# Kernel optimization log

Hardware: AMD Instinct MI355X
Metric: run time of the kernel (lower is better)

## Reference

```python
import jax, jax.numpy as jnp
import numpy as np

D_INPUT = 2048
DD_DIM = 512
DD_PAIRS = DD_DIM // 2


def setup_inputs() -> dict:
    key = jax.random.key(0)
    k1, k2, k3 = jax.random.split(key, 3)
    x = jax.random.normal(k1, (4, 4096, D_INPUT), dtype=jnp.float32)
    # Learned projection (zeros at init in torch; use small random for a non-trivial test)
    W = jax.random.normal(k2, (DD_PAIRS, D_INPUT), dtype=jnp.float32) * 0.02
    b = jax.random.normal(k3, (DD_PAIRS,), dtype=jnp.float32) * 0.02
    return {"x": x, "W": W, "b": b}


def reference(x, W, b):
    # x: (B, T, D); W: (P, D); b: (P,) with P = DD_DIM // 2
    deltas = jnp.einsum('btd,pd->btp', x, W) + b          # (B, T, P)
    angles = jnp.cumsum(deltas, axis=1)                   # cumulative phase
    cos, sin = jnp.cos(angles), jnp.sin(angles)
    x1 = x[..., :DD_PAIRS]                                # (B, T, P)
    x2 = x[..., DD_PAIRS:DD_DIM]                          # (B, T, P)
    rotated = jnp.concatenate([x1 * cos - x2 * sin, x2 * cos + x1 * sin], axis=-1)
    return jnp.concatenate([rotated, x[..., DD_DIM:]], axis=-1)
```

## Files before the change

kernel.cpp:

```cpp
#include <hip/hip_runtime.h>
#include <math.h>

#define BB 4
#define TT 4096
#define DDIM 2048
#define PP 256
#define MM (BB*TT)
#define KKDIM 2048
#define CHUNK 32
#define NCHUNK (TT/CHUNK)

typedef __attribute__((ext_vector_type(8))) short short8;
typedef __attribute__((ext_vector_type(4))) float f32x4;

__device__ __forceinline__ unsigned short f2bf(float f) {
    unsigned u = __float_as_uint(f);
    u += 0x7FFF + ((u >> 16) & 1);
    return (unsigned short)(u >> 16);
}
__device__ __forceinline__ float bf2f(unsigned short h) {
    return __uint_as_float(((unsigned)h) << 16);
}

#define LSTR 56

__global__ __launch_bounds__(256) void gemm_mfma_k(const float* __restrict__ x,
                                                   const float* __restrict__ W,
                                                   const float* __restrict__ bias,
                                                   float* __restrict__ delta,
                                                   float* __restrict__ csum) {
    __shared__ unsigned short Ahi[128 * LSTR];
    __shared__ unsigned short Alo[128 * LSTR];
    __shared__ unsigned short Bhi[64 * LSTR];
    __shared__ unsigned short Blo[64 * LSTR];

    const int n0   = blockIdx.x * 64;
    const int m0   = blockIdx.y * 128;
    const int tid  = threadIdx.x;
    const int w    = tid >> 6;
    const int lane = tid & 63;
    const int lm   = lane & 15;
    const int ko   = lane >> 4;

    f32x4 acc[2][4];
    #pragma unroll
    for (int i = 0; i < 2; ++i)
        #pragma unroll
        for (int j = 0; j < 4; ++j) {
            f32x4 z = {0.f, 0.f, 0.f, 0.f};
            acc[i][j] = z;
        }

    for (int k0 = 0; k0 < KKDIM; k0 += 32) {
        float4 av[4], bv[2];
        #pragma unroll
        for (int r = 0; r < 4; ++r) {
            int f = r * 256 + tid;
            av[r] = *(const float4*)(x + (size_t)(m0 + (f >> 3)) * KKDIM + k0 + ((f & 7) << 2));
        }
        #pragma unroll
        for (int r = 0; r < 2; ++r) {
            int f = r * 256 + tid;
            bv[r] = *(const float4*)(W + (size_t)(n0 + (f >> 3)) * KKDIM + k0 + ((f & 7) << 2));
        }
        __syncthreads();
        #pragma unroll
        for (int r = 0; r < 4; ++r) {
            int f = r * 256 + tid;
            int idx = (f >> 3) * LSTR + ((f & 7) << 2);
            float4 v = av[r];
            unsigned short h0 = f2bf(v.x), h1 = f2bf(v.y), h2 = f2bf(v.z), h3 = f2bf(v.w);
            unsigned short l0 = f2bf(v.x - bf2f(h0)), l1 = f2bf(v.y - bf2f(h1));
            unsigned short l2 = f2bf(v.z - bf2f(h2)), l3 = f2bf(v.w - bf2f(h3));
            uint2 hp = { (unsigned)h0 | ((unsigned)h1 << 16), (unsigned)h2 | ((unsigned)h3 << 16) };
            uint2 lp = { (unsigned)l0 | ((unsigned)l1 << 16), (unsigned)l2 | ((unsigned)l3 << 16) };
            *(uint2*)&Ahi[idx] = hp;
            *(uint2*)&Alo[idx] = lp;
        }
        #pragma unroll
        for (int r = 0; r < 2; ++r) {
            int f = r * 256 + tid;
            int idx = (f >> 3) * LSTR + ((f & 7) << 2);
            float4 v = bv[r];
            unsigned short h0 = f2bf(v.x), h1 = f2bf(v.y), h2 = f2bf(v.z), h3 = f2bf(v.w);
            unsigned short l0 = f2bf(v.x - bf2f(h0)), l1 = f2bf(v.y - bf2f(h1));
            unsigned short l2 = f2bf(v.z - bf2f(h2)), l3 = f2bf(v.w - bf2f(h3));
            uint2 hp = { (unsigned)h0 | ((unsigned)h1 << 16), (unsigned)h2 | ((unsigned)h3 << 16) };
            uint2 lp = { (unsigned)l0 | ((unsigned)l1 << 16), (unsigned)l2 | ((unsigned)l3 << 16) };
            *(uint2*)&Bhi[idx] = hp;
            *(uint2*)&Blo[idx] = lp;
        }
        __syncthreads();
        short8 ah[2], al[2], bh[4], bl[4];
        #pragma unroll
        for (int mt = 0; mt < 2; ++mt) {
            int idx = (w * 32 + mt * 16 + lm) * LSTR + ko * 8;
            ah[mt] = *(const short8*)&Ahi[idx];
            al[mt] = *(const short8*)&Alo[idx];
        }
        #pragma unroll
        for (int nt = 0; nt < 4; ++nt) {
            int idx = (nt * 16 + lm) * LSTR + ko * 8;
            bh[nt] = *(const short8*)&Bhi[idx];
            bl[nt] = *(const short8*)&Blo[idx];
        }
        #pragma unroll
        for (int mt = 0; mt < 2; ++mt)
            #pragma unroll
            for (int nt = 0; nt < 4; ++nt) {
                f32x4 c = acc[mt][nt];
                c = __builtin_amdgcn_mfma_f32_16x16x32_bf16(ah[mt], bh[nt], c, 0, 0, 0);
                c = __builtin_amdgcn_mfma_f32_16x16x32_bf16(ah[mt], bl[nt], c, 0, 0, 0);
                c = __builtin_amdgcn_mfma_f32_16x16x32_bf16(al[mt], bh[nt], c, 0, 0, 0);
                acc[mt][nt] = c;
            }
    }

    float bsv[4];
    #pragma unroll
    for (int nt = 0; nt < 4; ++nt) bsv[nt] = bias[n0 + nt * 16 + lm];

    float cs[4] = {0.f, 0.f, 0.f, 0.f};
    #pragma unroll
    for (int mt = 0; mt < 2; ++mt)
        #pragma unroll
        for (int nt = 0; nt < 4; ++nt)
            #pragma unroll
            for (int r = 0; r < 4; ++r) {
                float val = acc[mt][nt][r] + bsv[nt];
                int m = m0 + w * 32 + mt * 16 + ko * 4 + r;
                delta[(size_t)m * PP + n0 + nt * 16 + lm] = val;
                cs[nt] += val;
            }
    #pragma unroll
    for (int nt = 0; nt < 4; ++nt) {
        float s = cs[nt];
        s += __shfl_xor(s, 16);
        s += __shfl_xor(s, 32);
        if (lane < 16)
            csum[(size_t)(m0 / CHUNK + w) * PP + n0 + nt * 16 + lane] = s;
    }
}

__global__ __launch_bounds__(256) void scan_k(float* __restrict__ csum, int cstride) {
    const int idx = blockIdx.x * 256 + threadIdx.x;
    const int b = idx >> 8;
    const int p = idx & 255;
    float run = 0.f;
    for (int c0 = 0; c0 < NCHUNK; c0 += 8) {
        float v[8];
        #pragma unroll
        for (int j = 0; j < 8; ++j)
            v[j] = csum[(size_t)(b * NCHUNK + c0 + j) * cstride + p];
        #pragma unroll
        for (int j = 0; j < 8; ++j) {
            float t = v[j];
            csum[(size_t)(b * NCHUNK + c0 + j) * cstride + p] = run;
            run += t;
        }
    }
}

__global__ __launch_bounds__(256) void rotate_copy_k(const float* __restrict__ delta,
                                                     const float* __restrict__ csum,
                                                     const float* __restrict__ x,
                                                     float* __restrict__ out) {
    const int bc = blockIdx.x;
    const int p  = threadIdx.x;
    const int tbase = bc * CHUNK;
    float angle = csum[(size_t)bc * PP + p];
    for (int t = 0; t < CHUNK; ++t) {
        size_t row = (size_t)(tbase + t);
        angle += delta[row * PP + p];
        float s, co;
        sincosf(angle, &s, &co);
        float x1 = x[row * DDIM + p];
        float x2 = x[row * DDIM + PP + p];
        out[row * DDIM + p]      = x1 * co - x2 * s;
        out[row * DDIM + PP + p] = x2 * co + x1 * s;
    }
    const int half = p >> 7;
    const int q    = p & 127;
    for (int rp = 0; rp < 16; ++rp) {
        size_t row = (size_t)(tbase + rp * 2 + half);
        const float4* src = (const float4*)(x + row * DDIM + 512);
        float4*       dst = (float4*)(out + row * DDIM + 512);
        dst[q]       = src[q];
        dst[q + 128] = src[q + 128];
        dst[q + 256] = src[q + 256];
    }
}

__global__ __launch_bounds__(256) void gemm_k(const float* __restrict__ x,
                                              const float* __restrict__ W,
                                              const float* __restrict__ bias,
                                              float* __restrict__ delta,
                                              int dstride, int doff) {
    __shared__ float As[16][68];
    __shared__ float Bs[16][68];
    const int m0  = blockIdx.x * 64;
    const int n0  = blockIdx.y * 64;
    const int tid = threadIdx.x;
    const int lr  = tid >> 2;
    const int lc  = (tid & 3) << 2;
    const int tmi = tid & 15;
    const int tni = tid >> 4;
    float acc[4][4] = {};
    for (int k0 = 0; k0 < KKDIM; k0 += 16) {
        float4 a4 = *(const float4*)(x + (size_t)(m0 + lr) * KKDIM + k0 + lc);
        float4 b4 = *(const float4*)(W + (size_t)(n0 + lr) * KKDIM + k0 + lc);
        __syncthreads();
        As[lc + 0][lr] = a4.x; As[lc + 1][lr] = a4.y;
        As[lc + 2][lr] = a4.z; As[lc + 3][lr] = a4.w;
        Bs[lc + 0][lr] = b4.x; Bs[lc + 1][lr] = b4.y;
        Bs[lc + 2][lr] = b4.z; Bs[lc + 3][lr] = b4.w;
        __syncthreads();
        #pragma unroll
        for (int kk = 0; kk < 16; ++kk) {
            float4 av = *(const float4*)&As[kk][tmi * 4];
            float4 bv = *(const float4*)&Bs[kk][tni * 4];
            float am[4] = {av.x, av.y, av.z, av.w};
            float bn[4] = {bv.x, bv.y, bv.z, bv.w};
            #pragma unroll
            for (int i = 0; i < 4; ++i)
                #pragma unroll
                for (int j = 0; j < 4; ++j)
                    acc[i][j] += am[i] * bn[j];
        }
    }
    const float4 b4 = *(const float4*)(bias + n0 + tni * 4);
    #pragma unroll
    for (int i = 0; i < 4; ++i) {
        size_t m = (size_t)(m0 + tmi * 4 + i);
        float4 o;
        o.x = acc[i][0] + b4.x; o.y = acc[i][1] + b4.y;
        o.z = acc[i][2] + b4.z; o.w = acc[i][3] + b4.w;
        *(float4*)(delta + m * dstride + doff + n0 + tni * 4) = o;
    }
}

__global__ __launch_bounds__(256) void chunksum_k(const float* __restrict__ delta,
                                                  int dstride, int doff,
                                                  float* __restrict__ csum, int cstride) {
    const int bc = blockIdx.x;
    const int b  = bc / NCHUNK;
    const int c  = bc % NCHUNK;
    const int p  = threadIdx.x;
    const int tbase = b * TT + c * CHUNK;
    float s = 0.f;
    #pragma unroll 8
    for (int t = 0; t < CHUNK; ++t)
        s += delta[(size_t)(tbase + t) * dstride + doff + p];
    csum[(size_t)bc * cstride + p] = s;
}

__global__ __launch_bounds__(256) void rotate_k(const float* __restrict__ delta,
                                                int dstride, int doff,
                                                const float* __restrict__ csum, int cstride,
                                                const float* __restrict__ x,
                                                float* __restrict__ out) {
    const int bc = blockIdx.x;
    const int b  = bc / NCHUNK;
    const int c  = bc % NCHUNK;
    const int p  = threadIdx.x;
    const int tbase = b * TT + c * CHUNK;
    float angle = csum[(size_t)bc * cstride + p];
    for (int t = 0; t < CHUNK; ++t) {
        size_t row = (size_t)(tbase + t);
        angle += delta[row * dstride + doff + p];
        float s, co;
        sincosf(angle, &s, &co);
        float x1 = x[row * DDIM + p];
        float x2 = x[row * DDIM + PP + p];
        out[row * DDIM + p]      = x1 * co - x2 * s;
        out[row * DDIM + PP + p] = x2 * co + x1 * s;
    }
}

__global__ __launch_bounds__(256) void copy_k(const float* __restrict__ x,
                                              float* __restrict__ out) {
    const size_t row = (size_t)blockIdx.x * 4 + (threadIdx.x >> 6);
    const int lane = threadIdx.x & 63;
    const int col = 512 + (blockIdx.y * 64 + lane) * 4;
    const size_t a = row * DDIM + col;
    *(float4*)(out + a) = *(const float4*)(x + a);
}

extern "C" void kernel_launch(void* const* d_in, const int* in_sizes, int n_in,
                              void* d_out, int out_size, void* d_ws, size_t ws_size,
                              hipStream_t stream) {
    const float* x    = (const float*)d_in[0];
    const float* W    = (const float*)d_in[1];
    const float* bias = (const float*)d_in[2];
    float* out = (float*)d_out;

    const size_t delta_elems = (size_t)MM * PP;
    const size_t csum_elems  = (size_t)BB * NCHUNK * PP;
    const size_t need = (delta_elems + csum_elems) * sizeof(float);

    if (ws_size >= need) {
        float* delta = (float*)d_ws;
        float* csum  = (float*)d_ws + delta_elems;
        gemm_mfma_k<<<dim3(PP / 64, MM / 128), 256, 0, stream>>>(x, W, bias, delta, csum);
        scan_k<<<(BB * PP) / 256, 256, 0, stream>>>(csum, PP);
        rotate_copy_k<<<BB * NCHUNK, 256, 0, stream>>>(delta, csum, x, out);
    } else {
        float* delta = out; const int dstride = DDIM, doff = 512;
        float* csum  = out + 768; const int cstride = DDIM;
        gemm_k<<<dim3(MM / 64, PP / 64), 256, 0, stream>>>(x, W, bias, delta, dstride, doff);
        chunksum_k<<<BB * NCHUNK, 256, 0, stream>>>(delta, dstride, doff, csum, cstride);
        scan_k<<<(BB * PP) / 256, 256, 0, stream>>>(csum, cstride);
        rotate_k<<<BB * NCHUNK, 256, 0, stream>>>(delta, dstride, doff, csum, cstride, x, out);
        copy_k<<<dim3(MM / 4, 6), 256, 0, stream>>>(x, out);
    }
}
```

Measured before the change: 368.2 us.

## Pre-split inputs to bf16 hi/lo and add pipelined GEMM, LDS scan, fast rotate

Result: slower. 548.9 us (+49.1%).

```diff
diff --git a/kernel.cpp b/kernel.cpp
--- a/kernel.cpp
+++ b/kernel.cpp
@@ -20,6 +20,196 @@
 }
 __device__ __forceinline__ float bf2f(unsigned short h) {
     return __uint_as_float(((unsigned)h) << 16);
+}
+
+__global__ __launch_bounds__(256) void cvt_k(const float* __restrict__ src,
+                                             unsigned short* __restrict__ hi,
+                                             unsigned short* __restrict__ lo) {
+    size_t i = ((size_t)blockIdx.x * 256 + threadIdx.x) * 4;
+    float4 v = *(const float4*)(src + i);
+    unsigned short h0 = f2bf(v.x), h1 = f2bf(v.y), h2 = f2bf(v.z), h3 = f2bf(v.w);
+    unsigned short l0 = f2bf(v.x - bf2f(h0)), l1 = f2bf(v.y - bf2f(h1));
+    unsigned short l2 = f2bf(v.z - bf2f(h2)), l3 = f2bf(v.w - bf2f(h3));
+    uint2 hp = { (unsigned)h0 | ((unsigned)h1 << 16), (unsigned)h2 | ((unsigned)h3 << 16) };
+    uint2 lp = { (unsigned)l0 | ((unsigned)l1 << 16), (unsigned)l2 | ((unsigned)l3 << 16) };
+    *(uint2*)(hi + i) = hp;
+    *(uint2*)(lo + i) = lp;
+}
+
+#define LS 40
+
+__global__ __launch_bounds__(128) void gemm_bf16_k(
+        const unsigned short* __restrict__ xhi, const unsigned short* __restrict__ xlo,
+        const unsigned short* __restrict__ whi, const unsigned short* __restrict__ wlo,
+        const float* __restrict__ bias,
+        float* __restrict__ delta, float* __restrict__ csum) {
+    __shared__ unsigned short Ah[64 * LS], Al[64 * LS];
+    __shared__ unsigned short Bh[128 * LS], Bl[128 * LS];
+    const int n0   = blockIdx.x * 128;
+    const int m0   = blockIdx.y * 64;
+    const int tid  = threadIdx.x;
+    const int wn   = tid >> 6;
+    const int lane = tid & 63;
+    const int lm   = lane & 15;
+    const int ko   = lane >> 4;
+
+    f32x4 acc[4][4];
+    #pragma unroll
+    for (int i = 0; i < 4; ++i)
+        #pragma unroll
+        for (int j = 0; j < 4; ++j) {
+            f32x4 z = {0.f, 0.f, 0.f, 0.f};
+            acc[i][j] = z;
+        }
+
+    uint4 rah[2], ral[2], rbh[4], rbl[4];
+    auto load_tile = [&](int k0) {
+        #pragma unroll
+        for (int r = 0; r < 2; ++r) {
+            int slot = r * 128 + tid;
+            size_t g = (size_t)(m0 + (slot >> 2)) * KKDIM + k0 + ((slot & 3) << 3);
+            rah[r] = *(const uint4*)(xhi + g);
+            ral[r] = *(const uint4*)(xlo + g);
+        }
+        #pragma unroll
+        for (int r = 0; r < 4; ++r) {
+            int slot = r * 128 + tid;
+            size_t g = (size_t)(n0 + (slot >> 2)) * KKDIM + k0 + ((slot & 3) << 3);
+            rbh[r] = *(const uint4*)(whi + g);
+            rbl[r] = *(const uint4*)(wlo + g);
+        }
+    };
+    load_tile(0);
+
+    for (int k0 = 0; k0 < KKDIM; k0 += 32) {
+        __syncthreads();
+        #pragma unroll
+        for (int r = 0; r < 2; ++r) {
+            int slot = r * 128 + tid;
+            int idx = (slot >> 2) * LS + ((slot & 3) << 3);
+            *(uint4*)&Ah[idx] = rah[r];
+            *(uint4*)&Al[idx] = ral[r];
+        }
+        #pragma unroll
+        for (int r = 0; r < 4; ++r) {
+            int slot = r * 128 + tid;
+            int idx = (slot >> 2) * LS + ((slot & 3) << 3);
+            *(uint4*)&Bh[idx] = rbh[r];
+            *(uint4*)&Bl[idx] = rbl[r];
+        }
+        __syncthreads();
+        if (k0 + 32 < KKDIM) load_tile(k0 + 32);
+
+        short8 fah[4], fal[4], fbh[4], fbl[4];
+        #pragma unroll
+        for (int mt = 0; mt < 4; ++mt) {
+            int idx = (mt * 16 + lm) * LS + ko * 8;
+            fah[mt] = *(const short8*)&Ah[idx];
+            fal[mt] = *(const short8*)&Al[idx];
+        }
+        #pragma unroll
+        for (int nt = 0; nt < 4; ++nt) {
+            int idx = (wn * 64 + nt * 16 + lm) * LS + ko * 8;
+            fbh[nt] = *(const short8*)&Bh[idx];
+            fbl[nt] = *(const short8*)&Bl[idx];
+        }
+        #pragma unroll
+        for (int mt = 0; mt < 4; ++mt)
+            #pragma unroll
+            for (int nt = 0; nt < 4; ++nt) {
+                f32x4 c = acc[mt][nt];
+                c = __builtin_amdgcn_mfma_f32_16x16x32_bf16(fah[mt], fbh[nt], c, 0, 0, 0);
+                c = __builtin_amdgcn_mfma_f32_16x16x32_bf16(fah[mt], fbl[nt], c, 0, 0, 0);
+                c = __builtin_amdgcn_mfma_f32_16x16x32_bf16(fal[mt], fbh[nt], c, 0, 0, 0);
+                acc[mt][nt] = c;
+            }
+    }
+
+    float bs[4];
+    #pragma unroll
+    for (int nt = 0; nt < 4; ++nt) bs[nt] = bias[n0 + wn * 64 + nt * 16 + lm];
+
+    float cssum[2][4] = {};
+    #pragma unroll
+    for (int mt = 0; mt < 4; ++mt)
+        #pragma unroll
+        for (int nt = 0; nt < 4; ++nt)
+            #pragma unroll
+            for (int r = 0; r < 4; ++r) {
+                float val = acc[mt][nt][r] + bs[nt];
+                int m = m0 + mt * 16 + ko * 4 + r;
+                delta[(size_t)m * PP + n0 + wn * 64 + nt * 16 + lm] = val;
+                cssum[mt >> 1][nt] += val;
+            }
+    #pragma unroll
+    for (int c = 0; c < 2; ++c)
+        #pragma unroll
+        for (int nt = 0; nt < 4; ++nt) {
+            float s = cssum[c][nt];
+            s += __shfl_xor(s, 16);
+            s += __shfl_xor(s, 32);
+            if (lane < 16)
+                csum[(size_t)(blockIdx.y * 2 + c) * PP + n0 + wn * 64 + nt * 16 + lane] = s;
+        }
+}
+
+__global__ __launch_bounds__(256) void scan_lds_k(float* __restrict__ csum) {
+    __shared__ float s[2][128];
+    const int h = threadIdx.x >> 7, c = threadIdx.x & 127;
+    const int chain = blockIdx.x * 2 + h;
+    const int b = chain >> 8, p = chain & 255;
+    const size_t a = ((size_t)b * NCHUNK + c) * PP + p;
+    s[h][c] = csum[a];
+    __syncthreads();
+    for (int d = 1; d < 128; d <<= 1) {
+        float t = (c >= d) ? s[h][c - d] : 0.f;
+        __syncthreads();
+        s[h][c] += t;
+        __syncthreads();
+    }
+    csum[a] = (c == 0) ? 0.f : s[h][c - 1];
+}
+
+#define INV2PI 0.15915494309189535f
+
+__global__ __launch_bounds__(256) void rotate_copy_fast_k(const float* __restrict__ delta,
+                                                          const float* __restrict__ csum,
+                                                          const float* __restrict__ x,
+                                                          float* __restrict__ out) {
+    const int bc = blockIdx.x;
+    const int p  = threadIdx.x;
+    const int tbase = bc * CHUNK;
+    float d[CHUNK];
+    #pragma unroll
+    for (int t = 0; t < CHUNK; ++t)
+        d[t] = delta[(size_t)(tbase + t) * PP + p];
+    float angle = csum[(size_t)bc * PP + p];
+    float sn[CHUNK], cs[CHUNK];
+    #pragma unroll
+    for (int t = 0; t < CHUNK; ++t) {
+        angle += d[t];
+        float rev = angle * INV2PI;
+        sn[t] = __builtin_amdgcn_sinf(rev);
+        cs[t] = __builtin_amdgcn_cosf(rev);
+    }
+    #pragma unroll 8
+    for (int t = 0; t < CHUNK; ++t) {
+        size_t row = (size_t)(tbase + t);
+        float x1 = x[row * DDIM + p];
+        float x2 = x[row * DDIM + PP + p];
+        out[row * DDIM + p]      = x1 * cs[t] - x2 * sn[t];
+        out[row * DDIM + PP + p] = x2 * cs[t] + x1 * sn[t];
+    }
+    const int half = p >> 7;
+    const int q    = p & 127;
+    for (int rp = 0; rp < 16; ++rp) {
+        size_t row = (size_t)(tbase + rp * 2 + half);
+        const float4* src = (const float4*)(x + row * DDIM + 512);
+        float4*       dst = (float4*)(out + row * DDIM + 512);
+        dst[q]       = src[q];
+        dst[q + 128] = src[q + 128];
+        dst[q + 256] = src[q + 256];
+    }
 }
 
 #define LSTR 56
@@ -33,7 +223,6 @@
     __shared__ unsigned short Alo[128 * LSTR];
     __shared__ unsigned short Bhi[64 * LSTR];
     __shared__ unsigned short Blo[64 * LSTR];
-
     const int n0   = blockIdx.x * 64;
     const int m0   = blockIdx.y * 128;
     const int tid  = threadIdx.x;
@@ -119,7 +308,6 @@
     float bsv[4];
     #pragma unroll
     for (int nt = 0; nt < 4; ++nt) bsv[nt] = bias[n0 + nt * 16 + lm];
-
     float cs[4] = {0.f, 0.f, 0.f, 0.f};
     #pragma unroll
     for (int mt = 0; mt < 2; ++mt)
@@ -296,11 +484,26 @@
 
     const size_t delta_elems = (size_t)MM * PP;
     const size_t csum_elems  = (size_t)BB * NCHUNK * PP;
-    const size_t need = (delta_elems + csum_elems) * sizeof(float);
-
-    if (ws_size >= need) {
+    const size_t x_elems     = (size_t)MM * KKDIM;
+    const size_t w_elems     = (size_t)PP * KKDIM;
+    const size_t need2 = (delta_elems + csum_elems) * sizeof(float);
+    const size_t need1 = need2 + (2 * x_elems + 2 * w_elems) * sizeof(unsigned short);
+
+    if (ws_size >= need1) {
         float* delta = (float*)d_ws;
-        float* csum  = (float*)d_ws + delta_elems;
+        float* csum  = delta + delta_elems;
+        unsigned short* xhi = (unsigned short*)(csum + csum_elems);
+        unsigned short* xlo = xhi + x_elems;
+        unsigned short* whi = xlo + x_elems;
+        unsigned short* wlo = whi + w_elems;
+        cvt_k<<<x_elems / 1024, 256, 0, stream>>>(x, xhi, xlo);
+        cvt_k<<<w_elems / 1024, 256, 0, stream>>>(W, whi, wlo);
+        gemm_bf16_k<<<dim3(PP / 128, MM / 64), 128, 0, stream>>>(xhi, xlo, whi, wlo, bias, delta, csum);
+        scan_lds_k<<<(BB * PP) / 2, 256, 0, stream>>>(csum);
+        rotate_copy_fast_k<<<BB * NCHUNK, 256, 0, stream>>>(delta, csum, x, out);
+    } else if (ws_size >= need2) {
+        float* delta = (float*)d_ws;
+        float* csum  = delta + delta_elems;
         gemm_mfma_k<<<dim3(PP / 64, MM / 128), 256, 0, stream>>>(x, W, bias, delta, csum);
         scan_k<<<(BB * PP) / 256, 256, 0, stream>>>(csum, PP);
         rotate_copy_k<<<BB * NCHUNK, 256, 0, stream>>>(delta, csum, x, out);
```
